# Kernel optimization log

Hardware: AMD Instinct MI355X
Metric: run time of the kernel (lower is better)

Reference implementation:

```python
import jax, jax.numpy as jnp
import numpy as np

B, C, D = 16384, 4096, 512
ALPHA = 0.1
BETA = 0.25


def setup_inputs() -> dict:
    key = jax.random.key(0)
    kx, kc = jax.random.split(key)
    x = jax.random.normal(kx, (B, D), dtype=jnp.float32)
    codes = jax.random.normal(kc, (1, C, D), dtype=jnp.float32)
    return {"x": x, "codes": codes}


def reference(x, codes):
    # x: (B, D), codes: (1, C, D). Eval-mode forward of Quantizer (l2 metric).
    d = x.shape[1]
    c = codes[0]                                  # (C, D)
    # squared l2 distance via expansion (same math as sum((x-c)^2, -1))
    x_sq = jnp.sum(x * x, axis=-1, keepdims=True)  # (B, 1)
    c_sq = jnp.sum(c * c, axis=-1)                 # (C,)
    dots = jnp.einsum('bd,cd->bc', x, c)           # (B, C)
    raw_distances = x_sq + c_sq[None, :] - 2.0 * dots
    distances = raw_distances / d / ALPHA          # scaling preserved for faithfulness
    indices = jnp.argmin(distances, axis=-1)       # (B,)
    quantized = c[indices]                         # (B, D) gather
    # commit loss: dist(x, stop_grad(quantized)); codebook loss: dist(stop_grad(x), quantized)
    diff_commit = x - jax.lax.stop_gradient(quantized)
    loss_commit = jnp.mean(jnp.sum(diff_commit * diff_commit, axis=-1))
    diff_code = jax.lax.stop_gradient(x) - quantized
    loss_codebook = jnp.mean(jnp.sum(diff_code * diff_code, axis=-1))
    loss = loss_commit + BETA * loss_codebook
    return quantized, indices, loss
```

## Files before the change

### kernel.cpp

```cpp
#include <hip/hip_runtime.h>

#define B_SZ 16384
#define C_SZ 4096
#define D_SZ 512

#define QSCALE 22.7f
#define INV_S2 (1.0f / (QSCALE * QSCALE))
#define EPS 6.0f
#define DBIAS 1024.0f

typedef __attribute__((ext_vector_type(4))) int intx4;

__device__ inline unsigned q4(const float4 v) {
    int a = (int)rintf(v.x * QSCALE); a = max(-127, min(127, a));
    int b = (int)rintf(v.y * QSCALE); b = max(-127, min(127, b));
    int c = (int)rintf(v.z * QSCALE); c = max(-127, min(127, c));
    int d = (int)rintf(v.w * QSCALE); d = max(-127, min(127, d));
    return ((unsigned)(a & 255)) | ((unsigned)(b & 255) << 8) |
           ((unsigned)(c & 255) << 16) | ((unsigned)(d & 255) << 24);
}
__device__ inline void gload16(const void* g, void* l) {
    __builtin_amdgcn_global_load_lds(
        (const __attribute__((address_space(1))) void*)g,
        (__attribute__((address_space(3))) void*)l, 16, 0, 0);
}

#define ROR16(v, N) \
    ((unsigned)__builtin_amdgcn_update_dpp(0, (int)(v), 0x120 + (N), 0xF, 0xF, true))

__global__ __launch_bounds__(256) void convert_kernel(const float* __restrict__ x,
                                                      const float* __restrict__ codes,
                                                      unsigned* __restrict__ xq,
                                                      unsigned* __restrict__ cq,
                                                      float* __restrict__ csq,
                                                      float* __restrict__ xsq) {
    __shared__ float red[4];
    const int XB = (B_SZ * D_SZ) / 4 / 256;
    const int t = threadIdx.x;
    const int wave = t >> 6;
    const int lane = t & 63;
    if (blockIdx.x < XB) {
        const int tid = blockIdx.x * 256 + t;
        const float4 v = ((const float4*)x)[tid];
        xq[tid] = q4(v);
        float s = fmaf(v.x, v.x, fmaf(v.y, v.y, fmaf(v.z, v.z, v.w * v.w)));
        #pragma unroll
        for (int off = 32; off; off >>= 1) s += __shfl_down(s, off, 64);
        if (lane == 0) red[wave] = s;
        __syncthreads();
        if (t == 0) {
            xsq[blockIdx.x * 2]     = red[0] + red[1];
            xsq[blockIdx.x * 2 + 1] = red[2] + red[3];
        }
    } else {
        const int code = (blockIdx.x - XB) * 4 + wave;
        const float4* cp = (const float4*)(codes + (size_t)code * D_SZ);
        float s = 0.0f;
        #pragma unroll
        for (int u = 0; u < 2; ++u) {
            const float4 v = cp[lane + 64 * u];
            cq[(size_t)code * (D_SZ / 4) + lane + 64 * u] = q4(v);
            s = fmaf(v.x, v.x, s); s = fmaf(v.y, v.y, s);
            s = fmaf(v.z, v.z, s); s = fmaf(v.w, v.w, s);
        }
        #pragma unroll
        for (int off = 32; off; off >>= 1) s += __shfl_down(s, off, 64);
        if (lane == 0) csq[code] = s;
    }
}

__global__ __launch_bounds__(512, 4) void gemm_argmin_kernel(
        const unsigned char* __restrict__ xq,
        const unsigned char* __restrict__ cq,
        const float* __restrict__ csq,
        uint2* __restrict__ table) {
    __shared__ unsigned char sA[128][128];
    __shared__ unsigned char sB[256][128];

    const int t = threadIdx.x;
    const int wave = t >> 6;
    const int lane = t & 63;
    const int quad = lane >> 4;
    const int l15 = lane & 15;
    const int wm = wave >> 2;
    const int wn = wave & 3;

    const int rowbase = blockIdx.y * 128;
    const int colbase = blockIdx.x * 256;

    const int lrow = lane >> 3;
    const int lchunk = (lane & 7) ^ lrow;
    const unsigned char* gA = xq + (size_t)(rowbase + wave * 16 + lrow) * D_SZ + lchunk * 16;
    const unsigned char* gB = cq + (size_t)(colbase + wave * 32 + lrow) * D_SZ + lchunk * 16;

    float cs2[4];
    #pragma unroll
    for (int j = 0; j < 4; ++j)
        cs2[j] = fmaf(0.5f, csq[colbase + wn * 64 + j * 16 + l15], DBIAS);

    intx4 acc[4][4];
    #pragma unroll
    for (int i = 0; i < 4; ++i)
        #pragma unroll
        for (int j = 0; j < 4; ++j) acc[i][j] = (intx4)0;

    for (int kt = 0; kt < D_SZ / 128; ++kt) {
        const unsigned char* ga = gA + kt * 128;
        const unsigned char* gb = gB + kt * 128;
        gload16(ga,                    &sA[wave * 16][0]);
        gload16(ga + (size_t)8 * D_SZ, &sA[wave * 16 + 8][0]);
        #pragma unroll
        for (int u = 0; u < 4; ++u)
            gload16(gb + (size_t)(u * 8) * D_SZ, &sB[wave * 32 + u * 8][0]);
        __syncthreads();

        #pragma unroll
        for (int ksub = 0; ksub < 2; ++ksub) {
            const int cc = (((ksub * 4 + quad) ^ (l15 & 7))) * 16;
            intx4 a[4], b[4];
            #pragma unroll
            for (int i = 0; i < 4; ++i)
                a[i] = *(const intx4*)&sA[wm * 64 + i * 16 + l15][cc];
            #pragma unroll
            for (int j = 0; j < 4; ++j)
                b[j] = *(const intx4*)&sB[wn * 64 + j * 16 + l15][cc];
            #pragma unroll
            for (int i = 0; i < 4; ++i)
                #pragma unroll
                for (int j = 0; j < 4; ++j)
                    acc[i][j] = __builtin_amdgcn_mfma_i32_16x16x64_i8(a[i], b[j], acc[i][j], 0, 0, 0);
        }
        __syncthreads();
    }

    const int hb = blockIdx.x * 4 + wn;

#define MERGE_STEP(N) do { \
        const unsigned ok1 = ROR16(k1, N); \
        const unsigned ok2 = ROR16(k2, N); \
        const unsigned hi = max(k1, ok1); \
        const unsigned w2 = (k1 < ok1) ? k2 : ok2; \
        k1 = min(k1, ok1); \
        k2 = min(hi, w2); \
    } while (0)

    #pragma unroll
    for (int i = 0; i < 4; ++i) {
        #pragma unroll
        for (int r = 0; r < 4; ++r) {
            unsigned k[4];
            #pragma unroll
            for (int j = 0; j < 4; ++j) {
                const float d = fmaf(-(float)acc[i][j][r], INV_S2, cs2[j]);
                k[j] = (__float_as_uint(d) & 0xFFFFFFC0u) | (unsigned)(j * 16 + l15);
            }
            const unsigned lo1 = min(k[0], k[1]), hi1 = max(k[0], k[1]);
            const unsigned lo2 = min(k[2], k[3]), hi2 = max(k[2], k[3]);
            unsigned k1 = min(lo1, lo2);
            unsigned k2 = min(max(lo1, lo2), min(hi1, hi2));
            MERGE_STEP(8); MERGE_STEP(4); MERGE_STEP(2); MERGE_STEP(1);
            if (l15 == 0) {
                const int grow = rowbase + wm * 64 + i * 16 + quad * 4 + r;
                table[(size_t)grow * 64 + hb] = make_uint2(k1, k2);
            }
        }
    }
#undef MERGE_STEP
}

__global__ __launch_bounds__(256) void rerank_gather_loss_kernel(
        const float* __restrict__ x,
        const float* __restrict__ codes,
        const float* __restrict__ csq,
        const float* __restrict__ xsq,
        const uint2* __restrict__ table,
        float* __restrict__ outq,
        float* __restrict__ out_idx_f,
        float* __restrict__ loss_slot) {
    __shared__ float red[4];
    const int t = threadIdx.x;
    const int wave = t >> 6;
    const int lane = t & 63;
    const int row0 = (blockIdx.x * 4 + wave) * 4;

    uint2 e[4];
    #pragma unroll
    for (int r = 0; r < 4; ++r)
        e[r] = table[(size_t)(row0 + r) * 64 + lane];

    int fin[4];
    float wsum = 0.0f;
    #pragma unroll
    for (int r = 0; r < 4; ++r) {
        const unsigned k1 = e[r].x, k2 = e[r].y;
        unsigned mk = k1;
        #pragma unroll
        for (int off = 32; off; off >>= 1)
            mk = min(mk, (unsigned)__shfl_xor((int)mk, off, 64));

        const float thr = __uint_as_float(mk & 0xFFFFFFC0u) + EPS;
        const float v1 = __uint_as_float(k1 & 0xFFFFFFC0u);
        const float v2 = __uint_as_float(k2 & 0xFFFFFFC0u);
        const unsigned long long b1 = __ballot(v1 <= thr);
        const unsigned long long b2 = __ballot(v2 <= thr);

        const unsigned long long bm = __ballot(k1 == mk);
        fin[r] = (__ffsll(bm) - 1) * 64 + (int)(mk & 63u);
        float distp = __uint_as_float(mk & 0xFFFFFFC0u) - DBIAS;

        if (__popcll(b1) + __popcll(b2) > 1) {
            const float4* xp = (const float4*)(x + (size_t)(row0 + r) * D_SZ);
            const float4 xv0 = xp[lane];
            const float4 xv1 = xp[lane + 64];
            const int c1 = lane * 64 + (int)(k1 & 63u);
            const int c2 = lane * 64 + (int)(k2 & 63u);
            float bv = 3.4e38f; int bi = 0x7FFFFFFF;
            #pragma unroll
            for (int pass = 0; pass < 2; ++pass) {
                unsigned long long bb = pass ? b2 : b1;
                const int myc = pass ? c2 : c1;
                while (bb) {
                    const int src = __ffsll((unsigned long long)bb) - 1;
                    bb &= bb - 1;
                    const int ci = __shfl(myc, src, 64);
                    const float4* cp = (const float4*)(codes + (size_t)ci * D_SZ);
                    const float4 c0 = cp[lane];
                    const float4 c1v = cp[lane + 64];
                    float s = 0.0f;
                    s = fmaf(xv0.x, c0.x, s);  s = fmaf(xv0.y, c0.y, s);
                    s = fmaf(xv0.z, c0.z, s);  s = fmaf(xv0.w, c0.w, s);
                    s = fmaf(xv1.x, c1v.x, s); s = fmaf(xv1.y, c1v.y, s);
                    s = fmaf(xv1.z, c1v.z, s); s = fmaf(xv1.w, c1v.w, s);
                    #pragma unroll
                    for (int off = 32; off; off >>= 1) s += __shfl_xor(s, off, 64);
                    const float d = fmaf(0.5f, csq[ci], -s);
                    if (d < bv || (d == bv && ci < bi)) { bv = d; bi = ci; }
                }
            }
            fin[r] = bi;
            distp = bv;
        }
        wsum += xsq[row0 + r] + 2.0f * distp;
    }

    float4 qv[4][2];
    #pragma unroll
    for (int r = 0; r < 4; ++r) {
        const float4* qp = (const float4*)(codes + (size_t)fin[r] * D_SZ);
        qv[r][0] = qp[lane];
        qv[r][1] = qp[lane + 64];
    }

    #pragma unroll
    for (int r = 0; r < 4; ++r) {
        float4* op = (float4*)(outq + (size_t)(row0 + r) * D_SZ);
        op[lane] = qv[r][0];
        op[lane + 64] = qv[r][1];
        if (lane == 0) out_idx_f[row0 + r] = (float)fin[r];
    }

    if (lane == 0) red[wave] = wsum;
    __syncthreads();
    if (t == 0)
        atomicAdd(loss_slot, (red[0] + red[1] + red[2] + red[3]) * (1.25f / (float)B_SZ));
}

extern "C" void kernel_launch(void* const* d_in, const int* in_sizes, int n_in,
                              void* d_out, int out_size, void* d_ws, size_t ws_size,
                              hipStream_t stream) {
    const float* x = (const float*)d_in[0];
    const float* codes = (const float*)d_in[1];

    float* outq = (float*)d_out;
    float* out_idx_f = outq + (size_t)B_SZ * D_SZ;
    float* loss_slot = out_idx_f + B_SZ;

    unsigned char* xq = (unsigned char*)d_ws;
    unsigned char* cq = xq + (size_t)B_SZ * D_SZ;
    float* csq = (float*)(cq + (size_t)C_SZ * D_SZ);
    uint2* table = (uint2*)(csq + C_SZ);
    float* xsq = (float*)(table + (size_t)B_SZ * 64);

    const int XB = (B_SZ * D_SZ) / 4 / 256;
    const int CB = C_SZ / 4;
    convert_kernel<<<XB + CB, 256, 0, stream>>>(x, codes, (unsigned*)xq, (unsigned*)cq, csq, xsq);
    gemm_argmin_kernel<<<dim3(C_SZ / 256, B_SZ / 128), 512, 0, stream>>>(xq, cq, csq, table);
    rerank_gather_loss_kernel<<<B_SZ / 16, 256, 0, stream>>>(x, codes, csq, xsq, table, outq, out_idx_f, loss_slot);
}
```

Baseline: 165.9 us.

## Keep codebook tile resident in LDS across four row tiles with prefetched A

Each GEMM block now processes 512 rows instead of 128, holding the full 256x512 int8 codebook slice in LDS (loaded once during the first row tile) and reusing it across four row tiles. The next A k-slice is prefetched into LDS while the current one is computed from registers, with explicit waitcnt and sched barriers. The aim is to cut redundant codebook global loads and overlap loads with MFMA work. The cost is a much larger LDS footprint (160KB), occupancy reduced to one block per CU, and four times fewer blocks, which may leave CUs underused.

```diff
diff --git a/kernel.cpp b/kernel.cpp
--- a/kernel.cpp
+++ b/kernel.cpp
@@ -24,6 +24,10 @@
         (const __attribute__((address_space(1))) void*)g,
         (__attribute__((address_space(3))) void*)l, 16, 0, 0);
 }
+
+#define SCHEDB()  __builtin_amdgcn_sched_barrier(0)
+#define VM0()     do { SCHEDB(); asm volatile("s_waitcnt vmcnt(0)"); SCHEDB(); } while (0)
+#define LGKM0()   do { asm volatile("s_waitcnt lgkmcnt(0)"); SCHEDB(); } while (0)
 
 #define ROR16(v, N) \
     ((unsigned)__builtin_amdgcn_update_dpp(0, (int)(v), 0x120 + (N), 0xF, 0xF, true))
@@ -69,13 +73,13 @@
     }
 }
 
-__global__ __launch_bounds__(512, 4) void gemm_argmin_kernel(
+__global__ __launch_bounds__(512, 1) void gemm_argmin_kernel(
         const unsigned char* __restrict__ xq,
         const unsigned char* __restrict__ cq,
         const float* __restrict__ csq,
         uint2* __restrict__ table) {
+    __shared__ unsigned char sB[4][256][128];
     __shared__ unsigned char sA[128][128];
-    __shared__ unsigned char sB[256][128];
 
     const int t = threadIdx.x;
     const int wave = t >> 6;
@@ -85,56 +89,47 @@
     const int wm = wave >> 2;
     const int wn = wave & 3;
 
-    const int rowbase = blockIdx.y * 128;
+    const int rowbase0 = blockIdx.y * 512;
     const int colbase = blockIdx.x * 256;
 
     const int lrow = lane >> 3;
     const int lchunk = (lane & 7) ^ lrow;
-    const unsigned char* gA = xq + (size_t)(rowbase + wave * 16 + lrow) * D_SZ + lchunk * 16;
-    const unsigned char* gB = cq + (size_t)(colbase + wave * 32 + lrow) * D_SZ + lchunk * 16;
+    const unsigned char* gA0 = xq + (size_t)(rowbase0 + wave * 16 + lrow) * D_SZ + lchunk * 16;
+    const unsigned char* gB0 = cq + (size_t)(colbase + wave * 32 + lrow) * D_SZ + lchunk * 16;
 
     float cs2[4];
     #pragma unroll
     for (int j = 0; j < 4; ++j)
         cs2[j] = fmaf(0.5f, csq[colbase + wn * 64 + j * 16 + l15], DBIAS);
 
-    intx4 acc[4][4];
-    #pragma unroll
-    for (int i = 0; i < 4; ++i)
-        #pragma unroll
-        for (int j = 0; j < 4; ++j) acc[i][j] = (intx4)0;
-
-    for (int kt = 0; kt < D_SZ / 128; ++kt) {
-        const unsigned char* ga = gA + kt * 128;
-        const unsigned char* gb = gB + kt * 128;
-        gload16(ga,                    &sA[wave * 16][0]);
-        gload16(ga + (size_t)8 * D_SZ, &sA[wave * 16 + 8][0]);
-        #pragma unroll
-        for (int u = 0; u < 4; ++u)
-            gload16(gb + (size_t)(u * 8) * D_SZ, &sB[wave * 32 + u * 8][0]);
-        __syncthreads();
-
-        #pragma unroll
-        for (int ksub = 0; ksub < 2; ++ksub) {
-            const int cc = (((ksub * 4 + quad) ^ (l15 & 7))) * 16;
-            intx4 a[4], b[4];
-            #pragma unroll
-            for (int i = 0; i < 4; ++i)
-                a[i] = *(const intx4*)&sA[wm * 64 + i * 16 + l15][cc];
-            #pragma unroll
-            for (int j = 0; j < 4; ++j)
-                b[j] = *(const intx4*)&sB[wn * 64 + j * 16 + l15][cc];
-            #pragma unroll
-            for (int i = 0; i < 4; ++i)
-                #pragma unroll
-                for (int j = 0; j < 4; ++j)
-                    acc[i][j] = __builtin_amdgcn_mfma_i32_16x16x64_i8(a[i], b[j], acc[i][j], 0, 0, 0);
-        }
-        __syncthreads();
-    }
-
-    const int hb = blockIdx.x * 4 + wn;
-
+#define STAGE_A(rt, kt) do { \
+        const unsigned char* _g = gA0 + (size_t)(rt) * 128 * D_SZ + (kt) * 128; \
+        gload16(_g,                    &sA[wave * 16][0]); \
+        gload16(_g + (size_t)8 * D_SZ, &sA[wave * 16 + 8][0]); \
+    } while (0)
+#define STAGE_B(kt) do { \
+        const unsigned char* _g = gB0 + (kt) * 128; \
+        _Pragma("unroll") for (int u = 0; u < 4; ++u) \
+            gload16(_g + (size_t)(u * 8) * D_SZ, &sB[kt][wave * 32 + u * 8][0]); \
+    } while (0)
+#define LDA_REGS() do { \
+        _Pragma("unroll") for (int ks = 0; ks < 2; ++ks) { \
+            const int cc = (((ks * 4 + quad) ^ (l15 & 7))) * 16; \
+            _Pragma("unroll") for (int i = 0; i < 4; ++i) \
+                areg[ks][i] = *(const intx4*)&sA[wm * 64 + i * 16 + l15][cc]; \
+        } \
+    } while (0)
+#define COMPUTE_KT(kt) do { \
+        _Pragma("unroll") for (int ks = 0; ks < 2; ++ks) { \
+            const int cc = (((ks * 4 + quad) ^ (l15 & 7))) * 16; \
+            intx4 b[4]; \
+            _Pragma("unroll") for (int j = 0; j < 4; ++j) \
+                b[j] = *(const intx4*)&sB[kt][wn * 64 + j * 16 + l15][cc]; \
+            _Pragma("unroll") for (int i = 0; i < 4; ++i) \
+                _Pragma("unroll") for (int j = 0; j < 4; ++j) \
+                    acc[i][j] = __builtin_amdgcn_mfma_i32_16x16x64_i8(areg[ks][i], b[j], acc[i][j], 0, 0, 0); \
+        } \
+    } while (0)
 #define MERGE_STEP(N) do { \
         const unsigned ok1 = ROR16(k1, N); \
         const unsigned ok2 = ROR16(k2, N); \
@@ -144,27 +139,60 @@
         k2 = min(hi, w2); \
     } while (0)
 
-    #pragma unroll
-    for (int i = 0; i < 4; ++i) {
-        #pragma unroll
-        for (int r = 0; r < 4; ++r) {
-            unsigned k[4];
+    STAGE_B(0);
+    STAGE_A(0, 0);
+    VM0();
+    __syncthreads();
+
+    const int hb = blockIdx.x * 4 + wn;
+
+    for (int rt = 0; rt < 4; ++rt) {
+        intx4 acc[4][4];
+        #pragma unroll
+        for (int i = 0; i < 4; ++i)
             #pragma unroll
-            for (int j = 0; j < 4; ++j) {
-                const float d = fmaf(-(float)acc[i][j][r], INV_S2, cs2[j]);
-                k[j] = (__float_as_uint(d) & 0xFFFFFFC0u) | (unsigned)(j * 16 + l15);
+            for (int j = 0; j < 4; ++j) acc[i][j] = (intx4)0;
+
+        #pragma unroll
+        for (int kt = 0; kt < 4; ++kt) {
+            intx4 areg[2][4];
+            LDA_REGS();
+            LGKM0();
+            __syncthreads();
+            if (kt < 3) STAGE_A(rt, kt + 1);
+            else if (rt < 3) STAGE_A(rt + 1, 0);
+            if (rt == 0 && kt < 3) STAGE_B(kt + 1);
+            COMPUTE_KT(kt);
+            VM0();
+            __syncthreads();
+        }
+
+        #pragma unroll
+        for (int i = 0; i < 4; ++i) {
+            #pragma unroll
+            for (int r = 0; r < 4; ++r) {
+                unsigned k[4];
+                #pragma unroll
+                for (int j = 0; j < 4; ++j) {
+                    const float d = fmaf(-(float)acc[i][j][r], INV_S2, cs2[j]);
+                    k[j] = (__float_as_uint(d) & 0xFFFFFFC0u) | (unsigned)(j * 16 + l15);
+                }
+                const unsigned lo1 = min(k[0], k[1]), hi1 = max(k[0], k[1]);
+                const unsigned lo2 = min(k[2], k[3]), hi2 = max(k[2], k[3]);
+                unsigned k1 = min(lo1, lo2);
+                unsigned k2 = min(max(lo1, lo2), min(hi1, hi2));
+                MERGE_STEP(8); MERGE_STEP(4); MERGE_STEP(2); MERGE_STEP(1);
+                if (l15 == 0) {
+                    const int grow = rowbase0 + rt * 128 + wm * 64 + i * 16 + quad * 4 + r;
+                    table[(size_t)grow * 64 + hb] = make_uint2(k1, k2);
+                }
             }
-            const unsigned lo1 = min(k[0], k[1]), hi1 = max(k[0], k[1]);
-            const unsigned lo2 = min(k[2], k[3]), hi2 = max(k[2], k[3]);
-            unsigned k1 = min(lo1, lo2);
-            unsigned k2 = min(max(lo1, lo2), min(hi1, hi2));
-            MERGE_STEP(8); MERGE_STEP(4); MERGE_STEP(2); MERGE_STEP(1);
-            if (l15 == 0) {
-                const int grow = rowbase + wm * 64 + i * 16 + quad * 4 + r;
-                table[(size_t)grow * 64 + hb] = make_uint2(k1, k2);
-            }
-        }
-    }
+        }
+    }
+#undef STAGE_A
+#undef STAGE_B
+#undef LDA_REGS
+#undef COMPUTE_KT
 #undef MERGE_STEP
 }
 
@@ -284,6 +312,6 @@
     const int XB = (B_SZ * D_SZ) / 4 / 256;
     const int CB = C_SZ / 4;
     convert_kernel<<<XB + CB, 256, 0, stream>>>(x, codes, (unsigned*)xq, (unsigned*)cq, csq, xsq);
-    gemm_argmin_kernel<<<dim3(C_SZ / 256, B_SZ / 128), 512, 0, stream>>>(xq, cq, csq, table);
+    gemm_argmin_kernel<<<dim3(C_SZ / 256, B_SZ / 512), 512, 0, stream>>>(xq, cq, csq, table);
     rerank_gather_loss_kernel<<<B_SZ / 16, 256, 0, stream>>>(x, codes, csq, xsq, table, outq, out_idx_f, loss_slot);
 }
```

Result: no change. 167.4 us (+0.9%).
